# Performance work log

Hardware: AMD Instinct MI355X
Metric: run time of the kernel (lower is better)

The kernel has to match this reference:

```python
import jax, jax.numpy as jnp
import numpy as np

B, C, N, K = 8, 128, 4096, 16
EPS = 1e-5


def _bn(x, g, b, m, v):
    # eval-mode BatchNorm1d over channel dim of [B, C, N]
    scale = (g * jax.lax.rsqrt(v + EPS))[None, :, None]
    return x * scale + (b - m * g * jax.lax.rsqrt(v + EPS))[None, :, None]


def setup_inputs() -> dict:
    key = jax.random.key(0)
    ks = jax.random.split(key, 16)
    x = jax.random.normal(ks[0], (B, C, N), dtype=jnp.float32)
    # k incoming neighbors per node, src within the same batch graph
    src_local = jax.random.randint(ks[1], (B, N, K), 0, N)
    src = (src_local + jnp.arange(B, dtype=src_local.dtype)[:, None, None] * N).reshape(B * N, K)
    def u(k, shape, lo, hi):
        return jax.random.uniform(k, shape, jnp.float32, lo, hi)
    params = dict(
        W1=jax.random.normal(ks[2], (C, C), jnp.float32) * (1.0 / np.sqrt(C)),
        b1=jax.random.normal(ks[3], (C,), jnp.float32) * 0.02,
        g1=u(ks[4], (C,), 0.5, 1.5), be1=jax.random.normal(ks[5], (C,)) * 0.1,
        m1=jax.random.normal(ks[6], (C,)) * 0.1, v1=u(ks[7], (C,), 0.5, 1.5),
        Wmr=jax.random.normal(ks[8], (2 * C, 2 * C), jnp.float32) * (1.0 / np.sqrt(2 * C)),
        bmr=jax.random.normal(ks[9], (2 * C,), jnp.float32) * 0.02,
        W2=jax.random.normal(ks[10], (C, 2 * C), jnp.float32) * (1.0 / np.sqrt(2 * C)),
        b2=jax.random.normal(ks[11], (C,), jnp.float32) * 0.02,
        g2=u(ks[12], (C,), 0.5, 1.5), be2=jax.random.normal(ks[13], (C,)) * 0.1,
        m2=jax.random.normal(ks[14], (C,)) * 0.1, v2=u(ks[15], (C,), 0.5, 1.5),
    )
    return {"x": x, "src": src, **params}


def reference(x, src, W1, b1, g1, be1, m1, v1, Wmr, bmr, W2, b2, g2, be2, m2, v2):
    res = x
    # fc1: Conv1d(k=1) + BN, then ReLU
    h = jnp.einsum('oc,bcn->bon', W1, x) + b1[None, :, None]
    h = jax.nn.relu(_bn(h, g1, be1, m1, v1))
    # nodes: [B*N, C]
    xn = h.transpose(0, 2, 1).reshape(B * N, C)
    # MRConv: max over incoming edges of (dst - src) feature diff
    diff = xn[:, None, :] - xn[src]          # [B*N, K, C]
    max_diff = diff.max(axis=1)              # [B*N, C]
    cat = jnp.concatenate([xn, max_diff], axis=1)  # [B*N, 2C]
    hn = jax.nn.relu(cat @ Wmr.T + bmr)      # [B*N, 2C]
    h2 = hn.reshape(B, N, 2 * C).transpose(0, 2, 1)  # [B, 2C, N]
    # fc2: Conv1d(k=1) + BN
    out = jnp.einsum('oc,bcn->bon', W2, h2) + b2[None, :, None]
    out = _bn(out, g2, be2, m2, v2)
    out = out + res
    return jax.nn.relu(out)
```

## Files before the change

kernel.cpp:

```cpp
#include <hip/hip_runtime.h>


typedef short bf8_t __attribute__((ext_vector_type(8)));
typedef float f4_t  __attribute__((ext_vector_type(4)));

namespace {
constexpr int Bn = 8, Cc = 128, Nn = 4096, Kk = 16, C2 = 256;
constexpr int NODES = Bn * Nn;
constexpr float EPSf = 1e-5f;
}

__device__ __forceinline__ unsigned short f2bf(float f) {
    unsigned u = __float_as_uint(f);
    u += 0x7fffu + ((u >> 16) & 1u);
    return (unsigned short)(u >> 16);
}
__device__ __forceinline__ unsigned pk2(float a, float b) {
    return (unsigned)f2bf(a) | ((unsigned)f2bf(b) << 16);
}
__device__ __forceinline__ float bflo(unsigned u) { return __uint_as_float(u << 16); }
__device__ __forceinline__ float bfhi(unsigned u) { return __uint_as_float(u & 0xffff0000u); }
__device__ __forceinline__ unsigned diff2(unsigned o, unsigned m) {
    return pk2(bflo(o) - bflo(m), bfhi(o) - bfhi(m));
}

__device__ __forceinline__ bf8_t cvt_frag(const float* __restrict__ p) {
    const float4 a = *(const float4*)(p);
    const float4 b = *(const float4*)(p + 4);
    union { uint4 u; bf8_t f; } r;
    r.u.x = pk2(a.x, a.y);
    r.u.y = pk2(a.z, a.w);
    r.u.z = pk2(b.x, b.y);
    r.u.w = pk2(b.z, b.w);
    return r.f;
}

#define PKMIN(a, b) asm("v_pk_min_u16 %0, %0, %1" : "+v"(a) : "v"(b))

__global__ __launch_bounds__(512) void fc1_mfma(
    const float* __restrict__ x, const float* __restrict__ W1,
    const float* __restrict__ b1, const float* __restrict__ g1,
    const float* __restrict__ be1, const float* __restrict__ m1,
    const float* __restrict__ v1, const float* __restrict__ Wmr,
    const float* __restrict__ W2, ushort* __restrict__ Wmrbf,
    ushort* __restrict__ W2bf, ushort* __restrict__ xn)
{
    __shared__ __align__(16) ushort xS[64 * 136];
    __shared__ float scS[Cc], shS[Cc];
    const int t = threadIdx.x;
    const int bid = blockIdx.x;

    if (bid < 96) {
        const int e = bid * 1024 + t * 2;
        if (e < 65536) {
            const float2 v = *(const float2*)(Wmr + e);
            *(unsigned*)(Wmrbf + e) = pk2(v.x, v.y);
        } else {
            const float2 v = *(const float2*)(W2 + (e - 65536));
            *(unsigned*)(W2bf + (e - 65536)) = pk2(v.x, v.y);
        }
    }

    const int lb = (bid & 7) * 64 + (bid >> 3);
    const int node0 = lb * 64;
    const int b  = node0 >> 12;
    const int n0 = node0 & 4095;

    if (t < Cc) {
        const float s = g1[t] * rsqrtf(v1[t] + EPSf);
        scS[t] = s;
        shS[t] = (b1[t] - m1[t]) * s + be1[t];
    }

    {
        const int cp = t >> 3, q = t & 7;
        const float* p0 = x + ((size_t)(b * Cc + 2 * cp)) * Nn + n0 + q * 8;
        const float* p1 = p0 + Nn;
        const float4 a0 = *(const float4*)(p0);
        const float4 a1 = *(const float4*)(p0 + 4);
        const float4 c0 = *(const float4*)(p1);
        const float4 c1 = *(const float4*)(p1 + 4);
        ushort* base = xS + (size_t)q * 8 * 136 + ((cp * 2) ^ (q << 3));
        *(unsigned*)(base + 0 * 136) = pk2(a0.x, c0.x);
        *(unsigned*)(base + 1 * 136) = pk2(a0.y, c0.y);
        *(unsigned*)(base + 2 * 136) = pk2(a0.z, c0.z);
        *(unsigned*)(base + 3 * 136) = pk2(a0.w, c0.w);
        *(unsigned*)(base + 4 * 136) = pk2(a1.x, c1.x);
        *(unsigned*)(base + 5 * 136) = pk2(a1.y, c1.y);
        *(unsigned*)(base + 6 * 136) = pk2(a1.z, c1.z);
        *(unsigned*)(base + 7 * 136) = pk2(a1.w, c1.w);
    }
    __syncthreads();

    const int w = t >> 6, lane = t & 63;
    const int row16 = lane & 15, kg = lane >> 4;

    f4_t acc[4];
    const f4_t zero = {0.f, 0.f, 0.f, 0.f};
    #pragma unroll
    for (int j = 0; j < 4; ++j) acc[j] = zero;

    #pragma unroll
    for (int ks = 0; ks < 4; ++ks) {
        const int k0 = ks * 32 + kg * 8;
        const bf8_t aw = cvt_frag(W1 + (size_t)(w * 16 + row16) * Cc + k0);
        #pragma unroll
        for (int nsub = 0; nsub < 4; ++nsub) {
            const int n = nsub * 16 + row16;
            const bf8_t bx = *(const bf8_t*)(xS + n * 136 + (k0 ^ ((n >> 3) << 3)));
            acc[nsub] = __builtin_amdgcn_mfma_f32_16x16x32_bf16(aw, bx, acc[nsub], 0, 0, 0);
        }
    }

    const int o4 = w * 16 + kg * 4;
    const float s0 = scS[o4 + 0], s1 = scS[o4 + 1], s2 = scS[o4 + 2], s3 = scS[o4 + 3];
    const float h0 = shS[o4 + 0], h1 = shS[o4 + 1], h2 = shS[o4 + 2], h3 = shS[o4 + 3];
    #pragma unroll
    for (int nsub = 0; nsub < 4; ++nsub) {
        const int node = node0 + nsub * 16 + row16;
        float v0 = acc[nsub][0] * s0 + h0;
        float v1 = acc[nsub][1] * s1 + h1;
        float v2 = acc[nsub][2] * s2 + h2;
        float v3 = acc[nsub][3] * s3 + h3;
        v0 = v0 > 0.f ? v0 : 0.f;
        v1 = v1 > 0.f ? v1 : 0.f;
        v2 = v2 > 0.f ? v2 : 0.f;
        v3 = v3 > 0.f ? v3 : 0.f;
        uint2 pk;
        pk.x = pk2(v0, v1);
        pk.y = pk2(v2, v3);
        *(uint2*)(xn + (size_t)node * Cc + o4) = pk;
    }
}

__global__ __launch_bounds__(512) void mrfc2_mfma(
    const ushort* __restrict__ xn, const int* __restrict__ src,
    const ushort* __restrict__ Wmrbf, const float* __restrict__ bmr,
    const ushort* __restrict__ W2bf, const float* __restrict__ x,
    const float* __restrict__ b2, const float* __restrict__ g2,
    const float* __restrict__ be2, const float* __restrict__ m2,
    const float* __restrict__ v2, float* __restrict__ out)
{
    __shared__ __align__(16) ushort catS[64 * 264];
    __shared__ int srcS[64 * Kk];
    __shared__ float scS[Cc], shS[Cc];
    const int t = threadIdx.x;
    const int bid = blockIdx.x;
    const int lb = (bid & 7) * 64 + (bid >> 3);
    const int node0 = lb * 64;
    const int b  = node0 >> 12;
    const int n0 = node0 & 4095;

    if (t < Cc) {
        const float s = g2[t] * rsqrtf(v2[t] + EPSf);
        scS[t] = s;
        shS[t] = (b2[t] - m2[t]) * s + be2[t];
    }
    if (t < 256)
        ((int4*)srcS)[t] = ((const int4*)(src + (size_t)node0 * Kk))[t];
    __syncthreads();

    {
        const int nl = t >> 3, q = t & 7;
        const ushort* orow = xn + (size_t)(node0 + nl) * Cc + q * 16;
        uint4 ow0 = *(const uint4*)(orow + 0);
        uint4 ow1 = *(const uint4*)(orow + 8);
        const int* sl = srcS + nl * Kk;
        const ushort* sr = xn + (size_t)sl[0] * Cc + q * 16;
        uint4 mn0 = *(const uint4*)(sr + 0);
        uint4 mn1 = *(const uint4*)(sr + 8);
        #pragma unroll
        for (int k = 1; k < Kk; ++k) {
            const ushort* s = xn + (size_t)sl[k] * Cc + q * 16;
            uint4 v0 = *(const uint4*)(s + 0);
            uint4 v1 = *(const uint4*)(s + 8);
            PKMIN(mn0.x, v0.x); PKMIN(mn0.y, v0.y); PKMIN(mn0.z, v0.z); PKMIN(mn0.w, v0.w);
            PKMIN(mn1.x, v1.x); PKMIN(mn1.y, v1.y); PKMIN(mn1.z, v1.z); PKMIN(mn1.w, v1.w);
        }
        unsigned* crow = (unsigned*)(catS + nl * 264);
        *(uint4*)(crow + q * 8 + 0) = ow0;
        *(uint4*)(crow + q * 8 + 4) = ow1;
        uint4 d0, d1;
        d0.x = diff2(ow0.x, mn0.x); d0.y = diff2(ow0.y, mn0.y);
        d0.z = diff2(ow0.z, mn0.z); d0.w = diff2(ow0.w, mn0.w);
        d1.x = diff2(ow1.x, mn1.x); d1.y = diff2(ow1.y, mn1.y);
        d1.z = diff2(ow1.z, mn1.z); d1.w = diff2(ow1.w, mn1.w);
        *(uint4*)(crow + 64 + q * 8 + 0) = d0;
        *(uint4*)(crow + 64 + q * 8 + 4) = d1;
    }
    __syncthreads();

    const int w = t >> 6, lane = t & 63;
    const int row16 = lane & 15, kg = lane >> 4;

    const int jb = w * 32;
    {
        f4_t acc[2][4];
        const f4_t zero = {0.f, 0.f, 0.f, 0.f};
        #pragma unroll
        for (int i = 0; i < 2; ++i)
            #pragma unroll
            for (int j = 0; j < 4; ++j) acc[i][j] = zero;

        #pragma unroll
        for (int ks = 0; ks < 8; ++ks) {
            const int k0 = ks * 32 + kg * 8;
            bf8_t aw[2], bc[4];
            #pragma unroll
            for (int jsub = 0; jsub < 2; ++jsub)
                aw[jsub] = *(const bf8_t*)(Wmrbf + (size_t)(jb + jsub * 16 + row16) * C2 + k0);
            #pragma unroll
            for (int nsub = 0; nsub < 4; ++nsub)
                bc[nsub] = *(const bf8_t*)(catS + (nsub * 16 + row16) * 264 + k0);
            #pragma unroll
            for (int jsub = 0; jsub < 2; ++jsub)
                #pragma unroll
                for (int nsub = 0; nsub < 4; ++nsub)
                    acc[jsub][nsub] = __builtin_amdgcn_mfma_f32_16x16x32_bf16(
                        aw[jsub], bc[nsub], acc[jsub][nsub], 0, 0, 0);
        }
        __syncthreads();

        #pragma unroll
        for (int jsub = 0; jsub < 2; ++jsub) {
            const float4 bb = *(const float4*)(bmr + jb + jsub * 16 + kg * 4);
            #pragma unroll
            for (int nsub = 0; nsub < 4; ++nsub) {
                float v0 = acc[jsub][nsub][0] + bb.x;
                float v1 = acc[jsub][nsub][1] + bb.y;
                float v2_ = acc[jsub][nsub][2] + bb.z;
                float v3 = acc[jsub][nsub][3] + bb.w;
                v0 = v0 > 0.f ? v0 : 0.f;
                v1 = v1 > 0.f ? v1 : 0.f;
                v2_ = v2_ > 0.f ? v2_ : 0.f;
                v3 = v3 > 0.f ? v3 : 0.f;
                uint2 pk;
                pk.x = pk2(v0, v1);
                pk.y = pk2(v2_, v3);
                *(uint2*)(catS + (nsub * 16 + row16) * 264 + jb + jsub * 16 + kg * 4) = pk;
            }
        }
    }
    __syncthreads();

    {
        const int ob = w * 16;
        f4_t acc[4];
        const f4_t zero = {0.f, 0.f, 0.f, 0.f};
        #pragma unroll
        for (int j = 0; j < 4; ++j) acc[j] = zero;

        #pragma unroll
        for (int ks = 0; ks < 8; ++ks) {
            const int k0 = ks * 32 + kg * 8;
            const bf8_t aw = *(const bf8_t*)(W2bf + (size_t)(ob + row16) * C2 + k0);
            #pragma unroll
            for (int nsub = 0; nsub < 4; ++nsub) {
                const bf8_t bh = *(const bf8_t*)(catS + (nsub * 16 + row16) * 264 + k0);
                acc[nsub] = __builtin_amdgcn_mfma_f32_16x16x32_bf16(aw, bh, acc[nsub], 0, 0, 0);
            }
        }

        #pragma unroll
        for (int r = 0; r < 4; ++r) {
            const int o = ob + kg * 4 + r;
            const float s = scS[o], sh = shS[o];
            const float* xr = x   + ((size_t)(b * Cc + o)) * Nn + n0;
            float*       op = out + ((size_t)(b * Cc + o)) * Nn + n0;
            #pragma unroll
            for (int nsub = 0; nsub < 4; ++nsub) {
                const int nn = nsub * 16 + row16;
                float v = acc[nsub][r] * s + sh + xr[nn];
                v = v > 0.f ? v : 0.f;
                op[nn] = v;
            }
        }
    }
}

extern "C" void kernel_launch(void* const* d_in, const int* in_sizes, int n_in,
                              void* d_out, int out_size, void* d_ws, size_t ws_size,
                              hipStream_t stream)
{
    const float* x   = (const float*)d_in[0];
    const int*   src = (const int*)  d_in[1];
    const float* W1  = (const float*)d_in[2];
    const float* b1  = (const float*)d_in[3];
    const float* g1  = (const float*)d_in[4];
    const float* be1 = (const float*)d_in[5];
    const float* m1  = (const float*)d_in[6];
    const float* v1  = (const float*)d_in[7];
    const float* Wmr = (const float*)d_in[8];
    const float* bmr = (const float*)d_in[9];
    const float* W2  = (const float*)d_in[10];
    const float* b2  = (const float*)d_in[11];
    const float* g2  = (const float*)d_in[12];
    const float* be2 = (const float*)d_in[13];
    const float* m2  = (const float*)d_in[14];
    const float* v2  = (const float*)d_in[15];
    float* out = (float*)d_out;

    ushort* Wmrbf = (ushort*)d_ws;
    ushort* W2bf  = Wmrbf + 65536;
    ushort* xn    = W2bf + 32768;

    fc1_mfma<<<NODES / 64, 512, 0, stream>>>(x, W1, b1, g1, be1, m1, v1,
                                             Wmr, W2, Wmrbf, W2bf, xn);
    mrfc2_mfma<<<NODES / 64, 512, 0, stream>>>(xn, src, Wmrbf, bmr, W2bf, x,
                                               b2, g2, be2, m2, v2, out);
}
```

Measured before the change: 36.08 us.

## Prefetch residual tile into LDS and drop src staging barrier

The residual x tile is now loaded into registers with coalesced float4 reads at kernel start and staged in shared memory, so the epilogue reads LDS instead of issuing scattered global loads. The src indices are read straight into registers per thread, which removes the initial __syncthreads and srcS staging. The BN scale/shift setup moves after the first GEMM, reusing its existing barrier. The cost is 32KB more LDS per block, which may lower occupancy, plus higher register pressure.

```diff
diff --git a/kernel.cpp b/kernel.cpp
--- a/kernel.cpp
+++ b/kernel.cpp
@@ -142,7 +142,7 @@
     const float* __restrict__ v2, float* __restrict__ out)
 {
     __shared__ __align__(16) ushort catS[64 * 264];
-    __shared__ int srcS[64 * Kk];
+    __shared__ __align__(16) float xresS[128 * 64];
     __shared__ float scS[Cc], shS[Cc];
     const int t = threadIdx.x;
     const int bid = blockIdx.x;
@@ -151,21 +151,27 @@
     const int b  = node0 >> 12;
     const int n0 = node0 & 4095;
 
-    if (t < Cc) {
-        const float s = g2[t] * rsqrtf(v2[t] + EPSf);
-        scS[t] = s;
-        shS[t] = (b2[t] - m2[t]) * s + be2[t];
-    }
-    if (t < 256)
-        ((int4*)srcS)[t] = ((const int4*)(src + (size_t)node0 * Kk))[t];
-    __syncthreads();
+    const int xo = t >> 2, xseg = t & 3;
+    const float* xsrc = x + ((size_t)(b * Cc + xo)) * Nn + n0 + xseg * 16;
+    const float4 xr0 = ((const float4*)xsrc)[0];
+    const float4 xr1 = ((const float4*)xsrc)[1];
+    const float4 xr2 = ((const float4*)xsrc)[2];
+    const float4 xr3 = ((const float4*)xsrc)[3];
 
     {
         const int nl = t >> 3, q = t & 7;
-        const ushort* orow = xn + (size_t)(node0 + nl) * Cc + q * 16;
+        const int node = node0 + nl;
+        const int4 si0 = *(const int4*)(src + (size_t)node * Kk + 0);
+        const int4 si1 = *(const int4*)(src + (size_t)node * Kk + 4);
+        const int4 si2 = *(const int4*)(src + (size_t)node * Kk + 8);
+        const int4 si3 = *(const int4*)(src + (size_t)node * Kk + 12);
+        const int sl[16] = {si0.x, si0.y, si0.z, si0.w,
+                            si1.x, si1.y, si1.z, si1.w,
+                            si2.x, si2.y, si2.z, si2.w,
+                            si3.x, si3.y, si3.z, si3.w};
+        const ushort* orow = xn + (size_t)node * Cc + q * 16;
         uint4 ow0 = *(const uint4*)(orow + 0);
         uint4 ow1 = *(const uint4*)(orow + 8);
-        const int* sl = srcS + nl * Kk;
         const ushort* sr = xn + (size_t)sl[0] * Cc + q * 16;
         uint4 mn0 = *(const uint4*)(sr + 0);
         uint4 mn1 = *(const uint4*)(sr + 8);
@@ -188,6 +194,14 @@
         *(uint4*)(crow + 64 + q * 8 + 0) = d0;
         *(uint4*)(crow + 64 + q * 8 + 4) = d1;
     }
+
+    {
+        float* xd = xresS + xo * 64 + xseg * 16;
+        ((float4*)xd)[0] = xr0;
+        ((float4*)xd)[1] = xr1;
+        ((float4*)xd)[2] = xr2;
+        ((float4*)xd)[3] = xr3;
+    }
     __syncthreads();
 
     const int w = t >> 6, lane = t & 63;
@@ -218,6 +232,12 @@
                 for (int nsub = 0; nsub < 4; ++nsub)
                     acc[jsub][nsub] = __builtin_amdgcn_mfma_f32_16x16x32_bf16(
                         aw[jsub], bc[nsub], acc[jsub][nsub], 0, 0, 0);
+        }
+
+        if (t < Cc) {
+            const float s = g2[t] * rsqrtf(v2[t] + EPSf);
+            scS[t] = s;
+            shS[t] = (b2[t] - m2[t]) * s + be2[t];
         }
         __syncthreads();
 
@@ -265,12 +285,12 @@
         for (int r = 0; r < 4; ++r) {
             const int o = ob + kg * 4 + r;
             const float s = scS[o], sh = shS[o];
-            const float* xr = x   + ((size_t)(b * Cc + o)) * Nn + n0;
+            const float* xl = xresS + o * 64;
             float*       op = out + ((size_t)(b * Cc + o)) * Nn + n0;
             #pragma unroll
             for (int nsub = 0; nsub < 4; ++nsub) {
                 const int nn = nsub * 16 + row16;
-                float v = acc[nsub][r] * s + sh + xr[nn];
+                float v = acc[nsub][r] * s + sh + xl[nn];
                 v = v > 0.f ? v : 0.f;
                 op[nn] = v;
             }
```

Result: no change. 35.63 us, median of 2 (-1.2%).
